# Kernel tuning notes

Measured on AMD Instinct MI355X. Metric: run time of the kernel, lower is better.

The kernel has to match this reference:

```python
import jax, jax.numpy as jnp
import numpy as np

B, D, U = 8192, 512, 512


def setup_inputs() -> dict:
    key = jax.random.key(0)
    ks = jax.random.split(key, 5)
    return {
        "inputs": jax.random.normal(ks[0], (B, D), dtype=jnp.float32),
        "h_tm1": jax.random.normal(ks[1], (B, U), dtype=jnp.float32),
        "c_tm1": jax.random.normal(ks[2], (B, U), dtype=jnp.float32),
        "kernel": jax.random.normal(ks[3], (D, 4 * U), dtype=jnp.float32) * (1.0 / np.sqrt(D)),
        "recurrent_kernel": jax.random.normal(ks[4], (U, 4 * U), dtype=jnp.float32) * (1.0 / np.sqrt(U)),
        "bias": jnp.zeros((4 * U,), dtype=jnp.float32),
    }


def reference(inputs, h_tm1, c_tm1, kernel, recurrent_kernel, bias):
    # z: [B, 4U] = x @ W + h @ R + b
    z = inputs @ kernel + h_tm1 @ recurrent_kernel + bias
    z0, z1, z2, z3 = jnp.split(z, 4, axis=1)
    i = jax.nn.sigmoid(z0)
    f = jax.nn.sigmoid(z1)
    g = jnp.tanh(z2)
    o = jax.nn.sigmoid(z3)
    c = f * c_tm1 + i * g
    h = o * jnp.tanh(c)
    return (h, h, c)
```

## Files before the change

### kernel.cpp

```cpp
#include <hip/hip_runtime.h>
#include <hip/hip_bf16.h>
#include <cstdint>
#include <cstddef>

#define BB 8192
#define UU 512
#define KPACK 1024
#define NPACK 2048

using frag16 = __attribute__((ext_vector_type(8))) short;
using f32x4  = __attribute__((ext_vector_type(4))) float;

__device__ inline unsigned short f2bf(float f) {
  union { float f; unsigned u; } v; v.f = f;
  unsigned r = v.u + 0x7fffu + ((v.u >> 16) & 1u);
  return (unsigned short)(r >> 16);
}

__device__ inline float fast_sigmoid(float x) { return 1.0f / (1.0f + __expf(-x)); }
__device__ inline float fast_tanh(float x) {
  x = fminf(fmaxf(x, -15.f), 15.f);
  float e = __expf(-2.0f * x);
  return (1.0f - e) / (1.0f + e);
}

__global__ __launch_bounds__(256) void pack_kernel(const float* __restrict__ x,
                                                   const float* __restrict__ h,
                                                   const float* __restrict__ W,
                                                   const float* __restrict__ R,
                                                   short* __restrict__ Xp,
                                                   short* __restrict__ Bt) {
  if (blockIdx.x < 4096) {
    int idx = blockIdx.x * 256 + threadIdx.x;
    int row = idx >> 7;
    int k8  = (idx & 127) << 3;
    const float* src = (k8 < 512) ? (x + (size_t)row * 512 + k8)
                                  : (h + (size_t)row * 512 + (k8 - 512));
    float4 a = *(const float4*)(src);
    float4 b = *(const float4*)(src + 4);
    frag16 o;
    o[0] = f2bf(a.x); o[1] = f2bf(a.y); o[2] = f2bf(a.z); o[3] = f2bf(a.w);
    o[4] = f2bf(b.x); o[5] = f2bf(b.y); o[6] = f2bf(b.z); o[7] = f2bf(b.w);
    *(frag16*)(Xp + ((size_t)idx << 3)) = o;
  } else {
    __shared__ float tile[64][65];
    int b2 = blockIdx.x - 4096;
    int nb = (b2 & 31) * 64;
    int kb = (b2 >> 5) * 64;
    int t  = threadIdx.x;
#pragma unroll
    for (int rep = 0; rep < 16; ++rep) {
      int kr = rep * 4 + (t >> 6);
      int c  = t & 63;
      int kg = kb + kr;
      const float* s = (kg < 512) ? (W + (size_t)kg * 2048) : (R + (size_t)(kg - 512) * 2048);
      tile[c][kr] = s[nb + c];
    }
    __syncthreads();
#pragma unroll
    for (int rep = 0; rep < 4; ++rep) {
      int nn = rep * 16 + (t >> 4);
      int k4 = (t & 15) << 2;
      ushort4 o;
      o.x = f2bf(tile[nn][k4 + 0]);
      o.y = f2bf(tile[nn][k4 + 1]);
      o.z = f2bf(tile[nn][k4 + 2]);
      o.w = f2bf(tile[nn][k4 + 3]);
      *(ushort4*)(Bt + (size_t)(nb + nn) * 1024 + kb + k4) = o;
    }
  }
}

__global__ __launch_bounds__(256, 4) void lstm_mfma_kernel(
    const short* __restrict__ A,
    const short* __restrict__ Bt,
    const float* __restrict__ bias,
    const float* __restrict__ cprev,
    float* __restrict__ out)
{
  __shared__ short lds_a[128 * 64];
  __shared__ short lds_b[128 * 64];

  const int tid  = threadIdx.x;
  const int lane = tid & 63;
  const int wave = tid >> 6;
  const int wm = wave & 1, wn = wave >> 1;
  const int bm = blockIdx.x;
  const int bn = blockIdx.y;

  const int r8  = lane >> 3;
  const int kg  = lane & 7;
  const int kgx = kg ^ r8;

  const short* ga[4];
  const short* gb[4];
  int ls_off[4];
#pragma unroll
  for (int t = 0; t < 4; ++t) {
    int rowl = wave * 32 + t * 8 + r8;
    ga[t] = A + (size_t)(bm * 128 + rowl) * 1024 + kgx * 8;
    int u    = bn * 32 + ((rowl >> 6) << 4) + (rowl & 15);
    int gate = (rowl >> 4) & 3;
    gb[t] = Bt + (size_t)(gate * 512 + u) * 1024 + kgx * 8;
    ls_off[t] = (wave * 32 + t * 8) * 64;
  }

  const int q   = lane >> 4;
  const int c16 = lane & 15;
  const int mx  = c16 & 7;

  const int u = bn * 32 + wn * 16 + c16;
  const float b0 = bias[u];
  const float b1 = bias[512 + u];
  const float b2 = bias[1024 + u];
  const float b3 = bias[1536 + u];
  float cp[4][4];
#pragma unroll
  for (int i = 0; i < 4; ++i) {
    int row0 = bm * 128 + wm * 64 + i * 16 + q * 4;
#pragma unroll
    for (int r = 0; r < 4; ++r)
      cp[i][r] = cprev[(size_t)(row0 + r) * UU + u];
  }

  f32x4 acc[4][4];
#pragma unroll
  for (int i = 0; i < 4; ++i)
#pragma unroll
    for (int j = 0; j < 4; ++j)
      acc[i][j] = f32x4{0.f, 0.f, 0.f, 0.f};

  for (int kt = 0; kt < 16; ++kt) {
    const int k0 = kt * 64;
#pragma unroll
    for (int t = 0; t < 4; ++t)
      __builtin_amdgcn_global_load_lds(
          (const __attribute__((address_space(1))) void*)(ga[t] + k0),
          (__attribute__((address_space(3))) void*)(lds_a + ls_off[t]), 16, 0, 0);
#pragma unroll
    for (int t = 0; t < 4; ++t)
      __builtin_amdgcn_global_load_lds(
          (const __attribute__((address_space(1))) void*)(gb[t] + k0),
          (__attribute__((address_space(3))) void*)(lds_b + ls_off[t]), 16, 0, 0);
    __syncthreads();
#pragma unroll
    for (int s = 0; s < 2; ++s) {
      const int kch = (((s << 2) + q) ^ mx) << 3;
      frag16 af[4], bf[4];
#pragma unroll
      for (int i = 0; i < 4; ++i)
        af[i] = *(const frag16*)(lds_a + (wm * 64 + i * 16 + c16) * 64 + kch);
#pragma unroll
      for (int j = 0; j < 4; ++j)
        bf[j] = *(const frag16*)(lds_b + (wn * 64 + j * 16 + c16) * 64 + kch);
#pragma unroll
      for (int i = 0; i < 4; ++i)
#pragma unroll
        for (int j = 0; j < 4; ++j)
          acc[i][j] = __builtin_amdgcn_mfma_f32_16x16x32_bf16(af[i], bf[j], acc[i][j], 0, 0, 0);
    }
    __syncthreads();
  }

  float* outh0 = out;
  float* outh1 = out + (size_t)BB * UU;
  float* outc  = out + (size_t)2 * BB * UU;

#pragma unroll
  for (int i = 0; i < 4; ++i) {
    int row0 = bm * 128 + wm * 64 + i * 16 + q * 4;
#pragma unroll
    for (int r = 0; r < 4; ++r) {
      size_t off = (size_t)(row0 + r) * UU + u;
      float z0 = acc[i][0][r] + b0;
      float z1 = acc[i][1][r] + b1;
      float z2 = acc[i][2][r] + b2;
      float z3 = acc[i][3][r] + b3;
      float ig = fast_sigmoid(z0);
      float fg = fast_sigmoid(z1);
      float gg = fast_tanh(z2);
      float og = fast_sigmoid(z3);
      float cc = fg * cp[i][r] + ig * gg;
      float hh = og * fast_tanh(cc);
      outh0[off] = hh;
      outh1[off] = hh;
      outc[off]  = cc;
    }
  }
}

extern "C" void kernel_launch(void* const* d_in, const int* in_sizes, int n_in,
                              void* d_out, int out_size, void* d_ws, size_t ws_size,
                              hipStream_t stream) {
  const float* x  = (const float*)d_in[0];
  const float* h  = (const float*)d_in[1];
  const float* c  = (const float*)d_in[2];
  const float* W  = (const float*)d_in[3];
  const float* R  = (const float*)d_in[4];
  const float* b  = (const float*)d_in[5];
  float* out = (float*)d_out;

  short* Xp = (short*)d_ws;
  short* Bt = Xp + (size_t)BB * KPACK;

  pack_kernel<<<4608, 256, 0, stream>>>(x, h, W, R, Xp, Bt);
  lstm_mfma_kernel<<<dim3(64, 16), 256, 0, stream>>>(Xp, Bt, b, c, out);
}
```

Before: 160.2 us.

## Enlarge GEMM block tile to 256x128 with each wave owning 64 rows

The M tile grows from 128 to 256 rows per block. Each of the four waves now computes 64 rows across all 128 gate columns, so it holds a 4x8 accumulator grid, and the grid halves to 32x16 blocks. The previous-cell loads move from the prologue into the epilogue, and occupancy bounds drop from 4 to 2 blocks per CU. The aim is higher arithmetic intensity and less B-tile traffic per output. The cost is more registers, LDS and in-loop fragment loads, plus only 512 blocks on a 256-CU part, which risks low occupancy and a tail effect.

```diff
diff --git a/kernel.cpp b/kernel.cpp
--- a/kernel.cpp
+++ b/kernel.cpp
@@ -71,20 +71,19 @@
   }
 }
 
-__global__ __launch_bounds__(256, 4) void lstm_mfma_kernel(
+__global__ __launch_bounds__(256, 2) void lstm_mfma_kernel(
     const short* __restrict__ A,
     const short* __restrict__ Bt,
     const float* __restrict__ bias,
     const float* __restrict__ cprev,
     float* __restrict__ out)
 {
-  __shared__ short lds_a[128 * 64];
+  __shared__ short lds_a[256 * 64];
   __shared__ short lds_b[128 * 64];
 
   const int tid  = threadIdx.x;
   const int lane = tid & 63;
   const int wave = tid >> 6;
-  const int wm = wave & 1, wn = wave >> 1;
   const int bm = blockIdx.x;
   const int bn = blockIdx.y;
 
@@ -92,71 +91,62 @@
   const int kg  = lane & 7;
   const int kgx = kg ^ r8;
 
-  const short* ga[4];
+  const short* ga[8];
   const short* gb[4];
-  int ls_off[4];
+  int lsa_off[8], lsb_off[4];
+#pragma unroll
+  for (int t = 0; t < 8; ++t) {
+    int rowl = wave * 64 + t * 8 + r8;
+    ga[t] = A + (size_t)(bm * 256 + rowl) * 1024 + kgx * 8;
+    lsa_off[t] = (wave * 64 + t * 8) * 64;
+  }
 #pragma unroll
   for (int t = 0; t < 4; ++t) {
     int rowl = wave * 32 + t * 8 + r8;
-    ga[t] = A + (size_t)(bm * 128 + rowl) * 1024 + kgx * 8;
     int u    = bn * 32 + ((rowl >> 6) << 4) + (rowl & 15);
     int gate = (rowl >> 4) & 3;
     gb[t] = Bt + (size_t)(gate * 512 + u) * 1024 + kgx * 8;
-    ls_off[t] = (wave * 32 + t * 8) * 64;
+    lsb_off[t] = (wave * 32 + t * 8) * 64;
   }
 
   const int q   = lane >> 4;
   const int c16 = lane & 15;
   const int mx  = c16 & 7;
 
-  const int u = bn * 32 + wn * 16 + c16;
-  const float b0 = bias[u];
-  const float b1 = bias[512 + u];
-  const float b2 = bias[1024 + u];
-  const float b3 = bias[1536 + u];
-  float cp[4][4];
-#pragma unroll
-  for (int i = 0; i < 4; ++i) {
-    int row0 = bm * 128 + wm * 64 + i * 16 + q * 4;
-#pragma unroll
-    for (int r = 0; r < 4; ++r)
-      cp[i][r] = cprev[(size_t)(row0 + r) * UU + u];
-  }
-
-  f32x4 acc[4][4];
+  f32x4 acc[4][8];
 #pragma unroll
   for (int i = 0; i < 4; ++i)
 #pragma unroll
-    for (int j = 0; j < 4; ++j)
+    for (int j = 0; j < 8; ++j)
       acc[i][j] = f32x4{0.f, 0.f, 0.f, 0.f};
 
   for (int kt = 0; kt < 16; ++kt) {
     const int k0 = kt * 64;
 #pragma unroll
-    for (int t = 0; t < 4; ++t)
+    for (int t = 0; t < 8; ++t)
       __builtin_amdgcn_global_load_lds(
           (const __attribute__((address_space(1))) void*)(ga[t] + k0),
-          (__attribute__((address_space(3))) void*)(lds_a + ls_off[t]), 16, 0, 0);
+          (__attribute__((address_space(3))) void*)(lds_a + lsa_off[t]), 16, 0, 0);
 #pragma unroll
     for (int t = 0; t < 4; ++t)
       __builtin_amdgcn_global_load_lds(
           (const __attribute__((address_space(1))) void*)(gb[t] + k0),
-          (__attribute__((address_space(3))) void*)(lds_b + ls_off[t]), 16, 0, 0);
+          (__attribute__((address_space(3))) void*)(lds_b + lsb_off[t]), 16, 0, 0);
     __syncthreads();
 #pragma unroll
     for (int s = 0; s < 2; ++s) {
       const int kch = (((s << 2) + q) ^ mx) << 3;
-      frag16 af[4], bf[4];
+      frag16 af[4], bf[8];
 #pragma unroll
       for (int i = 0; i < 4; ++i)
-        af[i] = *(const frag16*)(lds_a + (wm * 64 + i * 16 + c16) * 64 + kch);
-#pragma unroll
-      for (int j = 0; j < 4; ++j)
-        bf[j] = *(const frag16*)(lds_b + (wn * 64 + j * 16 + c16) * 64 + kch);
+        af[i] = *(const frag16*)(lds_a + (wave * 64 + i * 16 + c16) * 64 + kch);
+#pragma unroll
+      for (int j = 0; j < 8; ++j)
+        bf[j] = *(const frag16*)(lds_b + (j * 16 + c16) * 64 + kch);
 #pragma unroll
       for (int i = 0; i < 4; ++i)
 #pragma unroll
-        for (int j = 0; j < 4; ++j)
+        for (int j = 0; j < 8; ++j)
           acc[i][j] = __builtin_amdgcn_mfma_f32_16x16x32_bf16(af[i], bf[j], acc[i][j], 0, 0, 0);
     }
     __syncthreads();
@@ -167,24 +157,33 @@
   float* outc  = out + (size_t)2 * BB * UU;
 
 #pragma unroll
-  for (int i = 0; i < 4; ++i) {
-    int row0 = bm * 128 + wm * 64 + i * 16 + q * 4;
-#pragma unroll
-    for (int r = 0; r < 4; ++r) {
-      size_t off = (size_t)(row0 + r) * UU + u;
-      float z0 = acc[i][0][r] + b0;
-      float z1 = acc[i][1][r] + b1;
-      float z2 = acc[i][2][r] + b2;
-      float z3 = acc[i][3][r] + b3;
-      float ig = fast_sigmoid(z0);
-      float fg = fast_sigmoid(z1);
-      float gg = fast_tanh(z2);
-      float og = fast_sigmoid(z3);
-      float cc = fg * cp[i][r] + ig * gg;
-      float hh = og * fast_tanh(cc);
-      outh0[off] = hh;
-      outh1[off] = hh;
-      outc[off]  = cc;
+  for (int uu = 0; uu < 2; ++uu) {
+    const int u = bn * 32 + uu * 16 + c16;
+    const float b0 = bias[u];
+    const float b1 = bias[512 + u];
+    const float b2 = bias[1024 + u];
+    const float b3 = bias[1536 + u];
+#pragma unroll
+    for (int i = 0; i < 4; ++i) {
+      int row0 = bm * 256 + wave * 64 + i * 16 + q * 4;
+#pragma unroll
+      for (int r = 0; r < 4; ++r) {
+        size_t off = (size_t)(row0 + r) * UU + u;
+        float z0 = acc[i][uu * 4 + 0][r] + b0;
+        float z1 = acc[i][uu * 4 + 1][r] + b1;
+        float z2 = acc[i][uu * 4 + 2][r] + b2;
+        float z3 = acc[i][uu * 4 + 3][r] + b3;
+        float ig = fast_sigmoid(z0);
+        float fg = fast_sigmoid(z1);
+        float gg = fast_tanh(z2);
+        float og = fast_sigmoid(z3);
+        float cp = cprev[off];
+        float cc = fg * cp + ig * gg;
+        float hh = og * fast_tanh(cc);
+        outh0[off] = hh;
+        outh1[off] = hh;
+        outc[off]  = cc;
+      }
     }
   }
 }
@@ -204,5 +203,5 @@
   short* Bt = Xp + (size_t)BB * KPACK;
 
   pack_kernel<<<4608, 256, 0, stream>>>(x, h, W, R, Xp, Bt);
-  lstm_mfma_kernel<<<dim3(64, 16), 256, 0, stream>>>(Xp, Bt, b, c, out);
-}
+  lstm_mfma_kernel<<<dim3(32, 16), 256, 0, stream>>>(Xp, Bt, b, c, out);
+}
```

New measurement: 153.5 us. 1.04x faster.
